# Kernel optimization log

Measured on AMD Instinct MI355X. Metric: run time of the kernel, lower is better.

The kernel has to match this reference:

```python
import jax, jax.numpy as jnp
import numpy as np

TOPN = 1000
MIN_SCORE = 0.05
NMS_THR = 0.5
MAX_OBJ = 100
B, A, C = 8, 100000, 80


def setup_inputs():
    key = jax.random.key(0)
    k1, k2, k3, k4 = jax.random.split(key, 4)
    cls_heads = jax.random.uniform(k1, (B, A, C), dtype=jnp.float32)  # sigmoid-like class scores
    reg_heads = (jax.random.normal(k2, (B, A, 4), dtype=jnp.float32) * 0.1)  # small tx,ty,tw,th
    ctr = jax.random.uniform(k3, (B, A, 2), minval=32.0, maxval=768.0)
    wh = jax.random.uniform(k4, (B, A, 2), minval=16.0, maxval=128.0)
    batch_anchors = jnp.concatenate([ctr - 0.5 * wh, ctr + 0.5 * wh], axis=-1)
    return {"cls_heads": cls_heads, "reg_heads": reg_heads, "batch_anchors": batch_anchors}


def _decode(reg, anchors):
    # snap tx,ty,tw,th to x1y1x2y2; original casts to int (truncation toward zero)
    awh = anchors[..., 2:4] - anchors[..., 0:2]
    actr = anchors[..., 0:2] + 0.5 * awh
    pwh = jnp.exp(reg[..., 2:4]) * awh
    pctr = reg[..., 0:2] * awh + actr
    boxes = jnp.concatenate([pctr - 0.5 * pwh, pctr + 0.5 * pwh], axis=-1)
    return jnp.trunc(boxes)  # matches torch .int() truncation, kept float


def _per_image(scores, classes, boxes):
    # score-threshold filter + descending sort + topn, done as masked top_k (fixed shapes)
    masked = jnp.where(scores > MIN_SCORE, scores, -jnp.inf)
    top_s, idx = jax.lax.top_k(masked, TOPN)
    valid = top_s > MIN_SCORE
    top_c = classes[idx].astype(jnp.float32)
    top_b = boxes[idx]  # [TOPN,4]

    # pairwise IoU (greedy python_nms math)
    wh = top_b[:, 2:4] - top_b[:, 0:2]
    area = jnp.clip(wh[:, 0] * wh[:, 1], 1e-4)  # clamp(min=0.0001)
    tl = jnp.maximum(top_b[:, None, 0:2], top_b[None, :, 0:2])
    br = jnp.minimum(top_b[:, None, 2:4], top_b[None, :, 2:4])
    sz = jnp.clip(br - tl, 0.0)
    inter = sz[..., 0] * sz[..., 1]
    union = jnp.clip(area[:, None] + area[None, :] - inter, 1e-4)
    iou = inter / union  # [TOPN,TOPN]

    ar = jnp.arange(TOPN)

    def body(i, supp):
        # box i, if not already suppressed, suppresses later boxes with iou >= thr
        return supp | ((~supp[i]) & (iou[i] >= NMS_THR) & (ar > i))

    supp = jax.lax.fori_loop(0, TOPN, body, ~valid)
    kept = (~supp) & valid

    # compact first MAX_OBJ kept detections (score order preserved); pad with -1 / zeros
    rank = jnp.cumsum(kept) - 1
    slot = jnp.where(kept & (rank < MAX_OBJ), rank, MAX_OBJ)  # dump slot MAX_OBJ
    out_s = jnp.full((MAX_OBJ + 1,), -1.0, jnp.float32).at[slot].set(jnp.where(kept, top_s, -1.0))[:MAX_OBJ]
    out_c = jnp.full((MAX_OBJ + 1,), -1.0, jnp.float32).at[slot].set(jnp.where(kept, top_c, -1.0))[:MAX_OBJ]
    out_b = jnp.zeros((MAX_OBJ + 1, 4), jnp.float32).at[slot].set(jnp.where(kept[:, None], top_b, 0.0))[:MAX_OBJ]
    return out_s, out_c, out_b


def reference(cls_heads, reg_heads, batch_anchors):
    scores = jnp.max(cls_heads, axis=2)        # [B,A]
    classes = jnp.argmax(cls_heads, axis=2)    # [B,A] int
    boxes = _decode(reg_heads, batch_anchors)  # [B,A,4]
    return jax.vmap(_per_image)(scores, classes, boxes)
```

## Files before the change

kernel.cpp:

```cpp
#include <hip/hip_runtime.h>
#include <cstdint>

#define NB 8
#define NA 100000
#define NC 80
#define TOPN 1000
#define MAXOBJ 100
#define CAND1 16384
#define SORTN 2048
#define MIN_SCORE 0.05f
#define NMS_THR 0.5f

__global__ __launch_bounds__(320) void k_scores(const float* __restrict__ cls,
                                                unsigned int* __restrict__ keys,
                                                int* __restrict__ clsid,
                                                unsigned long long* __restrict__ cand,
                                                unsigned int* __restrict__ n_cand) {
    __shared__ float sval[64 * 21];
    __shared__ int sidx[64 * 21];
    const int b = blockIdx.y;
    const int a0 = blockIdx.x * 64;
    const int t = threadIdx.x;
    const float4* base = (const float4*)(cls + ((size_t)b * NA + a0) * NC);
    const int fmax = (NA - a0) * 20 - 1;

    int f0 = t, f1 = 320 + t, f2 = 640 + t, f3 = 960 + t;
    float4 v0 = base[min(f0, fmax)];
    float4 v1 = base[min(f1, fmax)];
    float4 v2 = base[min(f2, fmax)];
    float4 v3 = base[min(f3, fmax)];

#define REDUCE4(v, f)                                                   \
    {                                                                   \
        float m = v.x; int ix = 0;                                      \
        if (v.y > m) { m = v.y; ix = 1; }                               \
        if (v.z > m) { m = v.z; ix = 2; }                               \
        if (v.w > m) { m = v.w; ix = 3; }                               \
        int al = (f) / 20, e = (f) % 20;                                \
        sval[al * 21 + e] = m;                                          \
        sidx[al * 21 + e] = e * 4 + ix;                                 \
    }
    REDUCE4(v0, f0) REDUCE4(v1, f1) REDUCE4(v2, f2) REDUCE4(v3, f3)
#undef REDUCE4
    __syncthreads();

    if (t < 64) {
        const int a = a0 + t;
        unsigned int key = 0u;
        if (a < NA) {
            float vm = sval[t * 21]; int vi = sidx[t * 21];
            for (int j = 1; j < 20; ++j) {
                float x = sval[t * 21 + j];
                if (x > vm) { vm = x; vi = sidx[t * 21 + j]; }
            }
            key = (vm > MIN_SCORE) ? __float_as_uint(vm) : 0u;
            size_t o = (size_t)b * NA + a;
            keys[o] = key;
            clsid[o] = vi;
        }
        const unsigned int T0 = __float_as_uint(0.999f);
        bool w = (a < NA) && (key >= T0);
        unsigned long long m = __ballot(w);
        if (m) {
            int leader = (int)__builtin_ctzll(m);
            unsigned int bs = 0;
            if (t == leader) bs = atomicAdd(&n_cand[b], (unsigned int)__popcll(m));
            bs = __shfl(bs, leader);
            unsigned int pos = bs + (unsigned int)__popcll(m & ((1ull << t) - 1ull));
            if (w && pos < CAND1)
                cand[(size_t)b * CAND1 + pos] =
                    ((unsigned long long)key << 32) |
                    (unsigned long long)(0xFFFFFFFFu - (unsigned int)a);
        }
    }
}

__device__ inline void wave_agg_hist(unsigned int* lh, int bin, bool pred) {
    unsigned long long active = __ballot(pred);
    const int lane = threadIdx.x & 63;
    while (active) {
        int leader = (int)__builtin_ctzll(active);
        int lbin = __shfl(bin, leader);
        unsigned long long mask = __ballot(pred && (bin == lbin));
        if (lane == leader) atomicAdd(&lh[lbin], (unsigned int)__popcll(mask));
        active &= ~mask;
    }
}

__device__ inline void top_threshold(const unsigned int* lh, int nbins, int minbin,
                                     unsigned int rank, int* out_bin, unsigned int* out_above) {
    const int lane = threadIdx.x;
    const int chunk = nbins >> 6;
    const int hi = nbins - 1 - lane * chunk;
    const int lo = hi - chunk + 1;
    unsigned int s = 0;
    for (int i = hi; i >= lo; --i)
        if (i >= minbin) s += lh[i];
    unsigned int incl = s;
    for (int d = 1; d < 64; d <<= 1) {
        unsigned int o = __shfl_up(incl, d);
        if (lane >= d) incl += o;
    }
    unsigned int pre = incl - s;
    bool hit = (pre < rank) && (incl >= rank);
    unsigned long long m = __ballot(hit);
    if (m == 0ull) {
        if (lane == 0) { *out_bin = -1; *out_above = 0; }
        return;
    }
    if (hit) {
        unsigned int cum = pre;
        int fb = -1;
        for (int i = hi; i >= lo; --i) {
            if (i < minbin) break;
            unsigned int c = lh[i];
            if (cum + c >= rank) { fb = i; break; }
            cum += c;
        }
        *out_bin = fb;
        *out_above = cum;
    }
}

__global__ __launch_bounds__(1024) void k_select(
    const unsigned int* __restrict__ keys, const int* __restrict__ clsid,
    const unsigned long long* __restrict__ cand, const unsigned int* __restrict__ n_cand,
    const float* __restrict__ reg, const float* __restrict__ anch,
    float* __restrict__ out) {
    __shared__ unsigned int lh[2048];
    __shared__ unsigned long long sk[SORTN];
    __shared__ float4 sbox[TOPN];
    __shared__ float ss[TOPN];
    __shared__ float scl[TOPN];
    __shared__ int s_bin;
    __shared__ unsigned int s_above;
    __shared__ unsigned int s_cnt;

    const int b = blockIdx.x;
    const int tid = threadIdx.x;
    const int lane = tid & 63;
    const unsigned int* kb = keys + (size_t)b * NA;
    const unsigned long long* cb = cand + (size_t)b * CAND1;
    float* out_s = out + b * MAXOBJ;
    float* out_c = out + NB * MAXOBJ + b * MAXOBJ;
    float* out_b = out + 2 * NB * MAXOBJ + b * MAXOBJ * 4;

    if (tid < MAXOBJ) { out_s[tid] = -1.0f; out_c[tid] = -1.0f; }
    if (tid < MAXOBJ * 4) out_b[tid] = 0.0f;

    const unsigned int n0 = n_cand[b];
    const bool fast = (n0 >= TOPN) && (n0 <= CAND1);
    const int N = fast ? (int)n0 : NA;

    for (int i = tid; i < 2048; i += 1024) lh[i] = 0;
    __syncthreads();
    for (int base = 0; base < N; base += 1024) {
        int i = base + tid;
        unsigned int k = 0u;
        if (i < N) k = fast ? (unsigned int)(cb[i] >> 32) : kb[i];
        wave_agg_hist(lh, (int)(k >> 21), (i < N) && (k != 0u));
    }
    __syncthreads();
    if (tid < 64) top_threshold(lh, 2048, 1, TOPN, &s_bin, &s_above);
    __syncthreads();
    const int p1 = s_bin;
    const unsigned int above1 = s_above;

    unsigned int T;
    if (p1 < 0) {
        T = 1u;
    } else {
        __syncthreads();
        for (int i = tid; i < 2048; i += 1024) lh[i] = 0;
        __syncthreads();
        for (int base = 0; base < N; base += 1024) {
            int i = base + tid;
            if (i < N) {
                unsigned int k = fast ? (unsigned int)(cb[i] >> 32) : kb[i];
                if ((int)(k >> 21) == p1) atomicAdd(&lh[(k >> 10) & 0x7FFu], 1u);
            }
        }
        __syncthreads();
        if (tid < 64) top_threshold(lh, 2048, 0, TOPN - above1, &s_bin, &s_above);
        __syncthreads();
        const int p2 = s_bin;
        const unsigned int above2 = above1 + s_above;
        if (p2 < 0) {
            T = 1u;
        } else {
            const unsigned int pref = ((unsigned int)p1 << 11) | (unsigned int)p2;
            __syncthreads();
            for (int i = tid; i < 1024; i += 1024) lh[i] = 0;
            __syncthreads();
            for (int base = 0; base < N; base += 1024) {
                int i = base + tid;
                if (i < N) {
                    unsigned int k = fast ? (unsigned int)(cb[i] >> 32) : kb[i];
                    if ((k >> 10) == pref) atomicAdd(&lh[k & 0x3FFu], 1u);
                }
            }
            __syncthreads();
            if (tid < 64) top_threshold(lh, 1024, 0, TOPN - above2, &s_bin, &s_above);
            __syncthreads();
            T = (s_bin < 0) ? 1u : ((pref << 10) | (unsigned int)s_bin);
        }
    }
    __syncthreads();

    for (int i = tid; i < SORTN; i += 1024) sk[i] = 0ull;
    if (tid == 0) s_cnt = 0;
    __syncthreads();
    for (int base = 0; base < N; base += 1024) {
        int i = base + tid;
        unsigned long long e = 0ull;
        unsigned int k = 0u;
        if (i < N) {
            if (fast) { e = cb[i]; k = (unsigned int)(e >> 32); }
            else {
                k = kb[i];
                e = ((unsigned long long)k << 32) |
                    (unsigned long long)(0xFFFFFFFFu - (unsigned int)i);
            }
        }
        bool w = (k >= T) && (k != 0u);
        unsigned long long m = __ballot(w);
        if (m) {
            int leader = (int)__builtin_ctzll(m);
            unsigned int bs = 0;
            if (lane == leader) bs = atomicAdd(&s_cnt, (unsigned int)__popcll(m));
            bs = __shfl(bs, leader);
            unsigned int pos = bs + (unsigned int)__popcll(m & ((1ull << lane) - 1ull));
            if (w && pos < SORTN) sk[pos] = e;
        }
    }
    __syncthreads();

    for (int k = 2; k <= SORTN; k <<= 1)
        for (int j = k >> 1; j > 0; j >>= 1) {
            __syncthreads();
            for (int i = tid; i < SORTN; i += 1024) {
                int ixj = i ^ j;
                if (ixj > i) {
                    unsigned long long x = sk[i], y = sk[ixj];
                    bool desc = ((i & k) == 0);
                    if (desc ? (x < y) : (x > y)) { sk[i] = y; sk[ixj] = x; }
                }
            }
        }
    __syncthreads();

    if (tid < TOPN) {
        unsigned long long e = sk[tid];
        unsigned int key = (unsigned int)(e >> 32);
        if (key != 0u) {
            int a = (int)(0xFFFFFFFFu - (unsigned int)e);
            size_t base = (size_t)b * NA + a;
            float4 r  = ((const float4*)reg)[base];
            float4 an = ((const float4*)anch)[base];
            float aw = an.z - an.x, ah = an.w - an.y;
            float acx = an.x + 0.5f * aw, acy = an.y + 0.5f * ah;
            float pw = expf(r.z) * aw, ph = expf(r.w) * ah;
            float pcx = r.x * aw + acx, pcy = r.y * ah + acy;
            float4 bx;
            bx.x = truncf(pcx - 0.5f * pw); bx.y = truncf(pcy - 0.5f * ph);
            bx.z = truncf(pcx + 0.5f * pw); bx.w = truncf(pcy + 0.5f * ph);
            sbox[tid] = bx;
            ss[tid] = __uint_as_float(key);
            scl[tid] = (float)clsid[base];
        } else {
            sbox[tid] = make_float4(0.f, 0.f, 0.f, 0.f);
            ss[tid] = -1.0f;
            scl[tid] = -1.0f;
        }
    }
    __syncthreads();
    if (tid >= 64) return;

    float k0x1 = 0, k0y1 = 0, k0x2 = 0, k0y2 = 0, k0a = 0;
    float k1x1 = 0, k1y1 = 0, k1x2 = 0, k1y2 = 0, k1a = 0;
    int kc = 0;
    for (int i = 0; i < TOPN; ++i) {
        float4 bi = sbox[i];
        float si = ss[i];
        if (!(si > MIN_SCORE)) break;
        float areai = fmaxf((bi.z - bi.x) * (bi.w - bi.y), 1e-4f);
        bool sup = false;
        if (lane < kc) {
            float ix = fminf(k0x2, bi.z) - fmaxf(k0x1, bi.x);
            float iy = fminf(k0y2, bi.w) - fmaxf(k0y1, bi.y);
            float inter = fmaxf(ix, 0.0f) * fmaxf(iy, 0.0f);
            float uni = fmaxf(k0a + areai - inter, 1e-4f);
            sup = (inter / uni) >= NMS_THR;
        }
        if (lane + 64 < kc) {
            float ix = fminf(k1x2, bi.z) - fmaxf(k1x1, bi.x);
            float iy = fminf(k1y2, bi.w) - fmaxf(k1y1, bi.y);
            float inter = fmaxf(ix, 0.0f) * fmaxf(iy, 0.0f);
            float uni = fmaxf(k1a + areai - inter, 1e-4f);
            sup = sup || ((inter / uni) >= NMS_THR);
        }
        if (__ballot(sup) == 0ull) {
            if (lane == 0) {
                out_s[kc] = si;
                out_c[kc] = scl[i];
                out_b[kc * 4 + 0] = bi.x; out_b[kc * 4 + 1] = bi.y;
                out_b[kc * 4 + 2] = bi.z; out_b[kc * 4 + 3] = bi.w;
            }
            if (kc < 64) {
                if (lane == kc) { k0x1 = bi.x; k0y1 = bi.y; k0x2 = bi.z; k0y2 = bi.w; k0a = areai; }
            } else {
                if (lane == kc - 64) { k1x1 = bi.x; k1y1 = bi.y; k1x2 = bi.z; k1y2 = bi.w; k1a = areai; }
            }
            ++kc;
            if (kc >= MAXOBJ) break;
        }
    }
}

extern "C" void kernel_launch(void* const* d_in, const int* in_sizes, int n_in,
                              void* d_out, int out_size, void* d_ws, size_t ws_size,
                              hipStream_t stream) {
    const float* cls  = (const float*)d_in[0];
    const float* reg  = (const float*)d_in[1];
    const float* anch = (const float*)d_in[2];
    float* out = (float*)d_out;
    char* ws = (char*)d_ws;

    unsigned int* keys = (unsigned int*)ws;
    int* clsid = (int*)(ws + 3200000);
    unsigned long long* cand = (unsigned long long*)(ws + 6400000);
    unsigned int* n_cand = (unsigned int*)(ws + 7448576);

    hipMemsetAsync(n_cand, 0, 32, stream);

    dim3 gscore((NA + 63) / 64, NB);
    k_scores<<<gscore, 320, 0, stream>>>(cls, keys, clsid, cand, n_cand);
    k_select<<<NB, 1024, 0, stream>>>(keys, clsid, cand, n_cand, reg, anch, out);
}
```

Before: 498.9 us.

## Shard candidate counters into padded per-region buckets to reduce atomic contention

The single per-image candidate counter is replaced by 64 region counters, each padded to its own 128-byte line, and each region gets a fixed 256-slot bucket. The score kernel picks a region from its block index, which spreads the global atomics that all blocks previously aimed at one address. The select kernel sums the region counts and, if no region overflowed and there are enough candidates, scans the fixed 16384-slot bucketed array while skipping slots past each region's count. The trade-off is that any region overflowing 256 entries sends that image down the slow full-array path, and the memset now clears more memory.

```diff
diff --git a/kernel.cpp b/kernel.cpp
--- a/kernel.cpp
+++ b/kernel.cpp
@@ -6,7 +6,9 @@
 #define NC 80
 #define TOPN 1000
 #define MAXOBJ 100
-#define CAND1 16384
+#define NREG 64
+#define REGCAP 256
+#define CTRSTRIDE 32
 #define SORTN 2048
 #define MIN_SCORE 0.05f
 #define NMS_THR 0.5f
@@ -62,13 +64,16 @@
         bool w = (a < NA) && (key >= T0);
         unsigned long long m = __ballot(w);
         if (m) {
+            const int r = blockIdx.x & (NREG - 1);
+            unsigned int* ctr = n_cand + (size_t)((b << 6) | r) * CTRSTRIDE;
+            unsigned long long* creg = cand + ((size_t)((b << 6) | r)) * REGCAP;
             int leader = (int)__builtin_ctzll(m);
             unsigned int bs = 0;
-            if (t == leader) bs = atomicAdd(&n_cand[b], (unsigned int)__popcll(m));
+            if (t == leader) bs = atomicAdd(ctr, (unsigned int)__popcll(m));
             bs = __shfl(bs, leader);
             unsigned int pos = bs + (unsigned int)__popcll(m & ((1ull << t) - 1ull));
-            if (w && pos < CAND1)
-                cand[(size_t)b * CAND1 + pos] =
+            if (w && pos < REGCAP)
+                creg[pos] =
                     ((unsigned long long)key << 32) |
                     (unsigned long long)(0xFFFFFFFFu - (unsigned int)a);
         }
@@ -132,15 +137,18 @@
     __shared__ float4 sbox[TOPN];
     __shared__ float ss[TOPN];
     __shared__ float scl[TOPN];
+    __shared__ unsigned int s_rc[NREG];
     __shared__ int s_bin;
     __shared__ unsigned int s_above;
     __shared__ unsigned int s_cnt;
+    __shared__ unsigned int s_tot;
+    __shared__ int s_ovf;
 
     const int b = blockIdx.x;
     const int tid = threadIdx.x;
     const int lane = tid & 63;
     const unsigned int* kb = keys + (size_t)b * NA;
-    const unsigned long long* cb = cand + (size_t)b * CAND1;
+    const unsigned long long* cb = cand + ((size_t)b << 6) * REGCAP;
     float* out_s = out + b * MAXOBJ;
     float* out_c = out + NB * MAXOBJ + b * MAXOBJ;
     float* out_b = out + 2 * NB * MAXOBJ + b * MAXOBJ * 4;
@@ -148,17 +156,44 @@
     if (tid < MAXOBJ) { out_s[tid] = -1.0f; out_c[tid] = -1.0f; }
     if (tid < MAXOBJ * 4) out_b[tid] = 0.0f;
 
-    const unsigned int n0 = n_cand[b];
-    const bool fast = (n0 >= TOPN) && (n0 <= CAND1);
-    const int N = fast ? (int)n0 : NA;
+    if (tid < NREG) {
+        unsigned int c = n_cand[(size_t)((b << 6) | tid) * CTRSTRIDE];
+        s_rc[tid] = c;
+        unsigned int cc = min(c, (unsigned int)REGCAP);
+        for (int d = 32; d; d >>= 1) cc += __shfl_down(cc, d);
+        unsigned long long om = __ballot(c > REGCAP);
+        if (tid == 0) { s_tot = cc; s_ovf = (om != 0ull) ? 1 : 0; }
+    }
+    __syncthreads();
+
+    const bool fast = (!s_ovf) && (s_tot >= TOPN);
+    const int N = fast ? (NREG * REGCAP) : NA;
+
+#define FETCH(i, k, e)                                                        \
+    {                                                                         \
+        (k) = 0u; (e) = 0ull;                                                 \
+        if ((i) < N) {                                                        \
+            if (fast) {                                                       \
+                int rr = (i) >> 8, pp = (i) & (REGCAP - 1);                   \
+                if (pp < (int)s_rc[rr]) {                                     \
+                    (e) = cb[i]; (k) = (unsigned int)((e) >> 32);             \
+                }                                                             \
+            } else {                                                          \
+                (k) = kb[i];                                                  \
+                (e) = ((unsigned long long)(k) << 32) |                       \
+                      (unsigned long long)(0xFFFFFFFFu - (unsigned int)(i));  \
+            }                                                                 \
+        }                                                                     \
+    }
 
     for (int i = tid; i < 2048; i += 1024) lh[i] = 0;
     __syncthreads();
     for (int base = 0; base < N; base += 1024) {
         int i = base + tid;
-        unsigned int k = 0u;
-        if (i < N) k = fast ? (unsigned int)(cb[i] >> 32) : kb[i];
-        wave_agg_hist(lh, (int)(k >> 21), (i < N) && (k != 0u));
+        unsigned int k; unsigned long long e;
+        FETCH(i, k, e)
+        (void)e;
+        wave_agg_hist(lh, (int)(k >> 21), k != 0u);
     }
     __syncthreads();
     if (tid < 64) top_threshold(lh, 2048, 1, TOPN, &s_bin, &s_above);
@@ -175,10 +210,10 @@
         __syncthreads();
         for (int base = 0; base < N; base += 1024) {
             int i = base + tid;
-            if (i < N) {
-                unsigned int k = fast ? (unsigned int)(cb[i] >> 32) : kb[i];
-                if ((int)(k >> 21) == p1) atomicAdd(&lh[(k >> 10) & 0x7FFu], 1u);
-            }
+            unsigned int k; unsigned long long e;
+            FETCH(i, k, e)
+            (void)e;
+            if (k != 0u && (int)(k >> 21) == p1) atomicAdd(&lh[(k >> 10) & 0x7FFu], 1u);
         }
         __syncthreads();
         if (tid < 64) top_threshold(lh, 2048, 0, TOPN - above1, &s_bin, &s_above);
@@ -194,10 +229,10 @@
             __syncthreads();
             for (int base = 0; base < N; base += 1024) {
                 int i = base + tid;
-                if (i < N) {
-                    unsigned int k = fast ? (unsigned int)(cb[i] >> 32) : kb[i];
-                    if ((k >> 10) == pref) atomicAdd(&lh[k & 0x3FFu], 1u);
-                }
+                unsigned int k; unsigned long long e;
+                FETCH(i, k, e)
+                (void)e;
+                if (k != 0u && (k >> 10) == pref) atomicAdd(&lh[k & 0x3FFu], 1u);
             }
             __syncthreads();
             if (tid < 64) top_threshold(lh, 1024, 0, TOPN - above2, &s_bin, &s_above);
@@ -212,16 +247,8 @@
     __syncthreads();
     for (int base = 0; base < N; base += 1024) {
         int i = base + tid;
-        unsigned long long e = 0ull;
-        unsigned int k = 0u;
-        if (i < N) {
-            if (fast) { e = cb[i]; k = (unsigned int)(e >> 32); }
-            else {
-                k = kb[i];
-                e = ((unsigned long long)k << 32) |
-                    (unsigned long long)(0xFFFFFFFFu - (unsigned int)i);
-            }
-        }
+        unsigned int k; unsigned long long e;
+        FETCH(i, k, e)
         bool w = (k >= T) && (k != 0u);
         unsigned long long m = __ballot(w);
         if (m) {
@@ -234,6 +261,7 @@
         }
     }
     __syncthreads();
+#undef FETCH
 
     for (int k = 2; k <= SORTN; k <<= 1)
         for (int j = k >> 1; j > 0; j >>= 1) {
@@ -331,7 +359,7 @@
     unsigned long long* cand = (unsigned long long*)(ws + 6400000);
     unsigned int* n_cand = (unsigned int*)(ws + 7448576);
 
-    hipMemsetAsync(n_cand, 0, 32, stream);
+    hipMemsetAsync(n_cand, 0, (size_t)NB * NREG * CTRSTRIDE * 4, stream);
 
     dim3 gscore((NA + 63) / 64, NB);
     k_scores<<<gscore, 320, 0, stream>>>(cls, keys, clsid, cand, n_cand);
```

New measurement: 449.8 us. 9.8% less time.
